# Optimization experiments

Measured on AMD Instinct MI355X. Metric: run time of the kernel, lower is better.

The kernel has to match this reference:

```python
import jax, jax.numpy as jnp
import numpy as np

B, S, H = 2, 2048, 1024
NH, HD = 16, 64  # num_heads, head_size


def setup_inputs() -> dict:
    key = jax.random.key(0)
    ks = jax.random.split(key, 8)
    return {
        "x": jax.random.normal(ks[0], (B, S, H), dtype=jnp.float32),
        "attn_mask": jax.random.randint(ks[1], (B, S, S), 0, 2, dtype=jnp.int32),
        "Wq": jax.random.normal(ks[2], (H, H), dtype=jnp.float32) * 0.02,
        "bq": jax.random.normal(ks[3], (H,), dtype=jnp.float32) * 0.02,
        "Wk": jax.random.normal(ks[4], (H, H), dtype=jnp.float32) * 0.02,
        "bk": jax.random.normal(ks[5], (H,), dtype=jnp.float32) * 0.02,
        "Wv": jax.random.normal(ks[6], (H, H), dtype=jnp.float32) * 0.02,
        "bv": jax.random.normal(ks[7], (H,), dtype=jnp.float32) * 0.02,
    }


def reference(x, attn_mask, Wq, bq, Wk, bk, Wv, bv):
    b, s, h = x.shape
    # QKV projections (self-attention: kv = attention_input)
    q = (jnp.einsum('bih,hx->bix', x, Wq) + bq).reshape(b, s, NH, HD)
    k = (jnp.einsum('bih,hx->bix', x, Wk) + bk).reshape(b, s, NH, HD)
    v = (jnp.einsum('bih,hx->bix', x, Wv) + bv).reshape(b, s, NH, HD)
    scale = 1.0 / (HD ** 0.5)
    # [B, NH, Sq, Skv] score matrix, additive mask, softmax
    attn_score = jnp.einsum('bind,bjnd->bnij', q, k) * scale
    adder = attn_mask.astype(jnp.float32)[:, None, :, :] * -10000.0
    attn_prob = jax.nn.softmax(attn_score + adder, axis=-1)
    # dropout is identity (training=False)
    attn_vec = jnp.einsum('bnij,bjnd->bind', attn_prob, v)
    return attn_vec.reshape(b, s, NH * HD)
```

## Files before the change

### kernel.cpp

```cpp
#include <hip/hip_runtime.h>
#include <hip/hip_bf16.h>
#include <math.h>


#define DI __device__ __forceinline__

typedef unsigned short u16;
typedef unsigned int u32;
typedef unsigned long long u64;
typedef __attribute__((ext_vector_type(8))) short bf16x8;
typedef __attribute__((ext_vector_type(4))) float f32x4;

constexpr int BB = 2, SS = 2048, HH = 1024, NHEAD = 16, HDIM = 64;

DI u16 f2bf(float f) {
  __hip_bfloat16 h = __float2bfloat16(f);
  union { __hip_bfloat16 h; u16 u; } c; c.h = h; return c.u;
}

DI void gload_lds16(const void* g, const void* l) {
  __builtin_amdgcn_global_load_lds(
      (const __attribute__((address_space(1))) u32*)(u64)g,
      (__attribute__((address_space(3))) u32*)(u32)(u64)l,
      16, 0, 0);
}

__global__ void xcast(const float* __restrict__ x, u16* __restrict__ xb) {
  const size_t i = ((size_t)blockIdx.x * 256 + threadIdx.x) * 8;
  float4 f0 = *(const float4*)(x + i);
  float4 f1 = *(const float4*)(x + i + 4);
  bf16x8 v;
  v[0] = (short)f2bf(f0.x); v[1] = (short)f2bf(f0.y);
  v[2] = (short)f2bf(f0.z); v[3] = (short)f2bf(f0.w);
  v[4] = (short)f2bf(f1.x); v[5] = (short)f2bf(f1.y);
  v[6] = (short)f2bf(f1.z); v[7] = (short)f2bf(f1.w);
  *(bf16x8*)(xb + i) = v;
}

__global__ void wtrans(const float* __restrict__ Wq, const float* __restrict__ Wk,
                       const float* __restrict__ Wv, u16* __restrict__ WT) {
  __shared__ u16 tile[64][65];
  const float* W = (blockIdx.z == 0) ? Wq : (blockIdx.z == 1) ? Wk : Wv;
  u16* Wt = WT + (size_t)blockIdx.z * HH * HH;
  const int n0 = blockIdx.x * 64, k0 = blockIdx.y * 64;
  for (int i = threadIdx.x; i < 64 * 64; i += 256) {
    int r = i >> 6, c = i & 63;
    tile[r][c] = f2bf(W[(size_t)(k0 + r) * HH + n0 + c]);
  }
  __syncthreads();
  for (int i = threadIdx.x; i < 64 * 64; i += 256) {
    int r = i >> 6, c = i & 63;
    Wt[(size_t)(n0 + r) * HH + k0 + c] = tile[c][r];
  }
}

__global__ void maskpack(const int* __restrict__ mask, u64* __restrict__ mb) {
  const size_t idx = (size_t)blockIdx.x * 256 + threadIdx.x;
  const int v = mask[idx];
  const u64 bal = __ballot(v != 0);
  if ((threadIdx.x & 63) == 0) mb[idx >> 6] = bal;
}

__global__ __launch_bounds__(256) void qkv_gemm(
    const u16* __restrict__ X, const u16* __restrict__ WTall,
    const float* __restrict__ bq, const float* __restrict__ bk,
    const float* __restrict__ bv,
    u16* __restrict__ Qo, u16* __restrict__ Ko, u16* __restrict__ Vo) {
  __shared__ alignas(128) u16 As[128 * 64];
  __shared__ alignas(128) u16 Bs[128 * 64];

  const int z = blockIdx.z;
  const u16* Wt = WTall + (size_t)z * HH * HH;
  const float* bias = (z == 0) ? bq : (z == 1) ? bk : bv;
  u16* Out = (z == 0) ? Qo : (z == 1) ? Ko : Vo;
  const float oscale = (z == 0) ? 0.18033688011112042f : 1.0f;

  const int tid = threadIdx.x;
  const int lane = tid & 63;
  const int w = tid >> 6;
  const int wm = (w >> 1) * 64, wn = (w & 1) * 64;
  const int lr = lane & 15, lkg = lane >> 4;
  const int m0 = blockIdx.y * 128, n0 = blockIdx.x * 128;

  u32 srow[4], scol[4];
#pragma unroll
  for (int i = 0; i < 4; ++i) {
    u32 f = i * 4096 + w * 1024 + lane * 16;
    u32 g = f ^ (((f >> 7) & 7) << 4);
    srow[i] = g >> 7;
    scol[i] = (g & 127) >> 1;
  }

  u32 aoff[4][2], boff[4][2];
#pragma unroll
  for (int mf = 0; mf < 4; ++mf)
#pragma unroll
    for (int ks = 0; ks < 2; ++ks) {
      int row = wm + mf * 16 + lr;
      aoff[mf][ks] = (u32)((row * 128 + ks * 64 + lkg * 16) ^ ((row & 7) << 4));
      row = wn + mf * 16 + lr;
      boff[mf][ks] = (u32)((row * 128 + ks * 64 + lkg * 16) ^ ((row & 7) << 4));
    }

  f32x4 acc[4][4];
#pragma unroll
  for (int i = 0; i < 4; ++i)
#pragma unroll
    for (int j = 0; j < 4; ++j) acc[i][j] = {0.f, 0.f, 0.f, 0.f};

  const u16* Xb = X + (size_t)m0 * HH;
  const u16* Wb = Wt + (size_t)n0 * HH;

  auto stage = [&](int kt) {
    const int k0 = kt * 64;
#pragma unroll
    for (int i = 0; i < 4; ++i) {
      gload_lds16(Xb + (size_t)srow[i] * HH + k0 + scol[i],
                  (const char*)As + i * 4096 + w * 1024);
      gload_lds16(Wb + (size_t)srow[i] * HH + k0 + scol[i],
                  (const char*)Bs + i * 4096 + w * 1024);
    }
  };

  stage(0);
  const int NT = HH / 64;
  for (int kt = 0; kt < NT; ++kt) {
    __syncthreads();
    bf16x8 a[2][4], bfr[2][4];
#pragma unroll
    for (int ks = 0; ks < 2; ++ks)
#pragma unroll
      for (int i = 0; i < 4; ++i) {
        a[ks][i] = *(const bf16x8*)((const char*)As + aoff[i][ks]);
        bfr[ks][i] = *(const bf16x8*)((const char*)Bs + boff[i][ks]);
      }
    __syncthreads();
    if (kt + 1 < NT) stage(kt + 1);
    __builtin_amdgcn_s_setprio(1);
#pragma unroll
    for (int ks = 0; ks < 2; ++ks)
#pragma unroll
      for (int mf = 0; mf < 4; ++mf)
#pragma unroll
        for (int nf = 0; nf < 4; ++nf)
          acc[mf][nf] = __builtin_amdgcn_mfma_f32_16x16x32_bf16(
              a[ks][mf], bfr[ks][nf], acc[mf][nf], 0, 0, 0);
    __builtin_amdgcn_s_setprio(0);
  }

#pragma unroll
  for (int mf = 0; mf < 4; ++mf)
#pragma unroll
    for (int nf = 0; nf < 4; ++nf) {
      const int gn = n0 + wn + nf * 16 + lr;
      const float bvv = bias[gn];
      const int nh = gn >> 6, hd = gn & 63;
#pragma unroll
      for (int r = 0; r < 4; ++r) {
        const int gm = m0 + wm + mf * 16 + lkg * 4 + r;
        const int bb = gm >> 11, ss = gm & 2047;
        const float v = (acc[mf][nf][r] + bvv) * oscale;
        if (z < 2)
          Out[(((size_t)bb * NHEAD + nh) * SS + ss) * HDIM + hd] = f2bf(v);
        else
          Out[(((size_t)bb * NHEAD + nh) * HDIM + hd) * SS + ss] = f2bf(v);
      }
    }
}

__global__ __launch_bounds__(256) void attn(
    const u16* __restrict__ Q, const u16* __restrict__ K,
    const u16* __restrict__ Vt, const u64* __restrict__ mb,
    float* __restrict__ out) {
  __shared__ alignas(128) u16 Ks[64 * 64];
  __shared__ alignas(128) u16 Vs[64 * 64];
  __shared__ alignas(128) u16 Ps[4][16][72];

  const int nh = blockIdx.x, qt = blockIdx.y, b = blockIdx.z;
  const int bnh = b * NHEAD + nh;
  const u16* Qh = Q + (size_t)bnh * SS * HDIM;
  const u16* Kh = K + (size_t)bnh * SS * HDIM;
  const u16* Vh = Vt + (size_t)bnh * HDIM * SS;
  const int q0 = qt * 64;

  const int tid = threadIdx.x, lane = tid & 63, w = tid >> 6;
  const int lr = lane & 15, lkg = lane >> 4;
  const int qrow_lane = q0 + w * 16 + lr;

  bf16x8 qf[2];
#pragma unroll
  for (int h = 0; h < 2; ++h)
    qf[h] = *(const bf16x8*)(Qh + (size_t)qrow_lane * HDIM + h * 32 + lkg * 8);

  u32 srow[2], scol[2];
#pragma unroll
  for (int i = 0; i < 2; ++i) {
    u32 f = i * 4096 + w * 1024 + lane * 16;
    u32 g = f ^ (((f >> 7) & 7) << 4);
    srow[i] = g >> 7;
    scol[i] = (g & 127) >> 1;
  }

  auto stage = [&](int t) {
    const int kv0 = t * 64;
#pragma unroll
    for (int i = 0; i < 2; ++i) {
      gload_lds16(Kh + (size_t)(kv0 + srow[i]) * HDIM + scol[i],
                  (const char*)Ks + i * 4096 + w * 1024);
      gload_lds16(Vh + (size_t)srow[i] * SS + kv0 + scol[i],
                  (const char*)Vs + i * 4096 + w * 1024);
    }
  };

  u32 koff[4][2];
#pragma unroll
  for (int i = 0; i < 4; ++i)
#pragma unroll
    for (int h = 0; h < 2; ++h) {
      int row = i * 16 + lr;
      koff[i][h] = (u32)((row * 128 + h * 64 + lkg * 16) ^ ((row & 7) << 4));
    }

  bf16x8 ones;
#pragma unroll
  for (int j = 0; j < 8; ++j) ones[j] = (short)0x3F80;

  f32x4 oacc[4];
  f32x4 lacc = {0.f, 0.f, 0.f, 0.f};
#pragma unroll
  for (int n = 0; n < 4; ++n) oacc[n] = {0.f, 0.f, 0.f, 0.f};

  stage(0);
  const int NT = SS / 64;
  for (int t = 0; t < NT; ++t) {
    __syncthreads();

    const u64 sh =
        mb[((size_t)b * SS + qrow_lane) * (SS / 64) + t] >> (lkg * 4);
    const u32 w01 = (u32)sh, w23 = (u32)(sh >> 32);

    f32x4 sacc[4];
#pragma unroll
    for (int kvb = 0; kvb < 4; ++kvb) sacc[kvb] = {0.f, 0.f, 0.f, 0.f};
    __builtin_amdgcn_s_setprio(1);
#pragma unroll
    for (int kvb = 0; kvb < 4; ++kvb)
#pragma unroll
      for (int h = 0; h < 2; ++h) {
        const bf16x8 kf = *(const bf16x8*)((const char*)Ks + koff[kvb][h]);
        sacc[kvb] = __builtin_amdgcn_mfma_f32_16x16x32_bf16(
            kf, qf[h], sacc[kvb], 0, 0, 0);
      }
    __builtin_amdgcn_s_setprio(0);

#pragma unroll
    for (int kvb = 0; kvb < 4; ++kvb) {
      const u32 word = (kvb < 2) ? w01 : w23;
      const int sb = (kvb & 1) * 16;
      union { u16 h[4]; u64 d; } pk;
#pragma unroll
      for (int r = 0; r < 4; ++r) {
        float s = sacc[kvb][r];
        s = ((word >> (sb + r)) & 1u) ? -14000.0f : s;
        pk.h[r] = f2bf(__builtin_amdgcn_exp2f(s));
      }
      *(u64*)&Ps[w][lr][kvb * 16 + lkg * 4] = pk.d;
    }

    __builtin_amdgcn_s_setprio(1);
#pragma unroll
    for (int ks = 0; ks < 2; ++ks) {
      const bf16x8 pf = *(const bf16x8*)&Ps[w][lr][ks * 32 + lkg * 8];
#pragma unroll
      for (int n = 0; n < 4; ++n) {
        const bf16x8 vf = *(const bf16x8*)((const char*)Vs + koff[n][ks]);
        oacc[n] = __builtin_amdgcn_mfma_f32_16x16x32_bf16(
            pf, vf, oacc[n], 0, 0, 0);
      }
      lacc = __builtin_amdgcn_mfma_f32_16x16x32_bf16(pf, ones, lacc, 0, 0, 0);
    }
    __builtin_amdgcn_s_setprio(0);

    __syncthreads();
    if (t + 1 < NT) stage(t + 1);
  }

#pragma unroll
  for (int r = 0; r < 4; ++r) {
    const float rcp = 1.0f / lacc[r];
    const int qrow = q0 + w * 16 + lkg * 4 + r;
#pragma unroll
    for (int n = 0; n < 4; ++n)
      out[((size_t)b * SS + qrow) * HH + nh * HDIM + n * 16 + lr] =
          oacc[n][r] * rcp;
  }
}

extern "C" void kernel_launch(void* const* d_in, const int* in_sizes, int n_in,
                              void* d_out, int out_size, void* d_ws,
                              size_t ws_size, hipStream_t stream) {
  const float* x = (const float*)d_in[0];
  const int* mask = (const int*)d_in[1];
  const float* Wq = (const float*)d_in[2];
  const float* bq = (const float*)d_in[3];
  const float* Wk = (const float*)d_in[4];
  const float* bk = (const float*)d_in[5];
  const float* Wv = (const float*)d_in[6];
  const float* bv = (const float*)d_in[7];
  float* out = (float*)d_out;

  char* ws = (char*)d_ws;
  const size_t MB = 1024 * 1024;
  u16* Qw = (u16*)(ws + 0 * MB);
  u16* Kw = (u16*)(ws + 8 * MB);
  u16* Vtw = (u16*)(ws + 16 * MB);
  u64* mbp = (u64*)(ws + 24 * MB);
  u16* Xb = (u16*)d_out;
  u16* WT = (u16*)((char*)d_out + 8 * MB);

  xcast<<<dim3((BB * SS * HH) / (256 * 8)), 256, 0, stream>>>(x, Xb);
  wtrans<<<dim3(16, 16, 3), 256, 0, stream>>>(Wq, Wk, Wv, WT);
  maskpack<<<dim3((BB * SS * SS) / 256), 256, 0, stream>>>(mask, mbp);
  qkv_gemm<<<dim3(8, 32, 3), 256, 0, stream>>>(Xb, WT, bq, bk, bv, Qw, Kw, Vtw);
  attn<<<dim3(NHEAD, SS / 64, BB), 256, 0, stream>>>(Qw, Kw, Vtw, mbp, out);
}
```

Measured before the change: 133.8 us.

## Load K/V fragments directly from global into registers, dropping LDS staging

The attention kernel no longer stages K and V tiles into shared memory with async global-to-LDS loads and block barriers. Each wave now loads its own MFMA K and V fragments straight from global memory into registers, prefetching K one tile ahead, and both __syncthreads calls are gone. Launch bounds now request 4 blocks per CU to raise occupancy. The trade-off is that every wave re-reads the same K/V data, so global/L1 traffic is about four times higher. V is loaded in the same iteration it is used, leaving little latency hiding, and the final K prefetch reads past the end of the tile range.

Result: slower. 314.2 us (+134.8%).

```diff
diff --git a/kernel.cpp b/kernel.cpp
--- a/kernel.cpp
+++ b/kernel.cpp
@@ -168,13 +168,13 @@
     }
 }
 
-__global__ __launch_bounds__(256) void attn(
+__global__ __launch_bounds__(256, 4) void attn(
     const u16* __restrict__ Q, const u16* __restrict__ K,
     const u16* __restrict__ Vt, const u64* __restrict__ mb,
     float* __restrict__ out) {
-  __shared__ alignas(128) u16 Ks[64 * 64];
-  __shared__ alignas(128) u16 Vs[64 * 64];
-  __shared__ alignas(128) u16 Ps[4][16][72];
+  __shared__ alignas(16) u16 Ps[4][16][72];
+
+  const int tid = threadIdx.x, lane = tid & 63, w = tid >> 6;
 
   const int nh = blockIdx.x, qt = blockIdx.y, b = blockIdx.z;
   const int bnh = b * NHEAD + nh;
@@ -183,7 +183,6 @@
   const u16* Vh = Vt + (size_t)bnh * HDIM * SS;
   const int q0 = qt * 64;
 
-  const int tid = threadIdx.x, lane = tid & 63, w = tid >> 6;
   const int lr = lane & 15, lkg = lane >> 4;
   const int qrow_lane = q0 + w * 16 + lr;
 
@@ -192,35 +191,6 @@
   for (int h = 0; h < 2; ++h)
     qf[h] = *(const bf16x8*)(Qh + (size_t)qrow_lane * HDIM + h * 32 + lkg * 8);
 
-  u32 srow[2], scol[2];
-#pragma unroll
-  for (int i = 0; i < 2; ++i) {
-    u32 f = i * 4096 + w * 1024 + lane * 16;
-    u32 g = f ^ (((f >> 7) & 7) << 4);
-    srow[i] = g >> 7;
-    scol[i] = (g & 127) >> 1;
-  }
-
-  auto stage = [&](int t) {
-    const int kv0 = t * 64;
-#pragma unroll
-    for (int i = 0; i < 2; ++i) {
-      gload_lds16(Kh + (size_t)(kv0 + srow[i]) * HDIM + scol[i],
-                  (const char*)Ks + i * 4096 + w * 1024);
-      gload_lds16(Vh + (size_t)srow[i] * SS + kv0 + scol[i],
-                  (const char*)Vs + i * 4096 + w * 1024);
-    }
-  };
-
-  u32 koff[4][2];
-#pragma unroll
-  for (int i = 0; i < 4; ++i)
-#pragma unroll
-    for (int h = 0; h < 2; ++h) {
-      int row = i * 16 + lr;
-      koff[i][h] = (u32)((row * 128 + h * 64 + lkg * 16) ^ ((row & 7) << 4));
-    }
-
   bf16x8 ones;
 #pragma unroll
   for (int j = 0; j < 8; ++j) ones[j] = (short)0x3F80;
@@ -230,13 +200,34 @@
 #pragma unroll
   for (int n = 0; n < 4; ++n) oacc[n] = {0.f, 0.f, 0.f, 0.f};
 
-  stage(0);
+  bf16x8 kf[4][2], vf[4][2];
+  const u16* Kfl = Kh + (size_t)lr * HDIM + lkg * 8;
+  const u16* Vfl = Vh + (size_t)lr * SS + lkg * 8;
+
+  auto loadK = [&](int t) {
+    const u16* base = Kfl + (size_t)t * 64 * HDIM;
+#pragma unroll
+    for (int i = 0; i < 4; ++i)
+#pragma unroll
+      for (int h = 0; h < 2; ++h)
+        kf[i][h] = *(const bf16x8*)(base + (size_t)i * 16 * HDIM + h * 32);
+  };
+  auto loadV = [&](int t) {
+    const u16* base = Vfl + t * 64;
+#pragma unroll
+    for (int n = 0; n < 4; ++n)
+#pragma unroll
+      for (int h = 0; h < 2; ++h)
+        vf[n][h] = *(const bf16x8*)(base + (size_t)n * 16 * SS + h * 32);
+  };
+
+  const u64* mrow = mb + ((size_t)b * SS + qrow_lane) * (SS / 64);
+
+  loadK(0);
   const int NT = SS / 64;
   for (int t = 0; t < NT; ++t) {
-    __syncthreads();
-
-    const u64 sh =
-        mb[((size_t)b * SS + qrow_lane) * (SS / 64) + t] >> (lkg * 4);
+    loadV(t);
+    const u64 sh = mrow[t] >> (lkg * 4);
     const u32 w01 = (u32)sh, w23 = (u32)(sh >> 32);
 
     f32x4 sacc[4];
@@ -246,12 +237,12 @@
 #pragma unroll
     for (int kvb = 0; kvb < 4; ++kvb)
 #pragma unroll
-      for (int h = 0; h < 2; ++h) {
-        const bf16x8 kf = *(const bf16x8*)((const char*)Ks + koff[kvb][h]);
+      for (int h = 0; h < 2; ++h)
         sacc[kvb] = __builtin_amdgcn_mfma_f32_16x16x32_bf16(
-            kf, qf[h], sacc[kvb], 0, 0, 0);
-      }
+            kf[kvb][h], qf[h], sacc[kvb], 0, 0, 0);
     __builtin_amdgcn_s_setprio(0);
+
+    loadK(t + 1);
 
 #pragma unroll
     for (int kvb = 0; kvb < 4; ++kvb) {
@@ -272,17 +263,12 @@
     for (int ks = 0; ks < 2; ++ks) {
       const bf16x8 pf = *(const bf16x8*)&Ps[w][lr][ks * 32 + lkg * 8];
 #pragma unroll
-      for (int n = 0; n < 4; ++n) {
-        const bf16x8 vf = *(const bf16x8*)((const char*)Vs + koff[n][ks]);
+      for (int n = 0; n < 4; ++n)
         oacc[n] = __builtin_amdgcn_mfma_f32_16x16x32_bf16(
-            pf, vf, oacc[n], 0, 0, 0);
-      }
+            pf, vf[n][ks], oacc[n], 0, 0, 0);
       lacc = __builtin_amdgcn_mfma_f32_16x16x32_bf16(pf, ones, lacc, 0, 0, 0);
     }
     __builtin_amdgcn_s_setprio(0);
-
-    __syncthreads();
-    if (t + 1 < NT) stage(t + 1);
   }
 
 #pragma unroll
```

## Split attention KV range across two wave groups and combine partials in LDS

Applied to the files above, without the earlier changes.

The attention block grows from 256 to 512 threads. Each half of the waves processes half of the KV sequence for the same 64 query rows, each with its own K/V LDS tiles. At the end the second group writes its unnormalized output and row-sum partials to shared memory, and the first group adds them and normalizes. This is split-K within a block, meant to double the parallelism per query tile and halve the serial loop length. The cost is more LDS per block, which may lower occupancy, plus an extra combine step. The combine is valid without max rescaling because the kernel uses no running max.

After: 132.0 us. About the same (-1.3%).

```diff
diff --git a/kernel.cpp b/kernel.cpp
--- a/kernel.cpp
+++ b/kernel.cpp
@@ -168,13 +168,16 @@
     }
 }
 
-__global__ __launch_bounds__(256) void attn(
+__global__ __launch_bounds__(512) void attn(
     const u16* __restrict__ Q, const u16* __restrict__ K,
     const u16* __restrict__ Vt, const u64* __restrict__ mb,
     float* __restrict__ out) {
-  __shared__ alignas(128) u16 Ks[64 * 64];
-  __shared__ alignas(128) u16 Vs[64 * 64];
-  __shared__ alignas(128) u16 Ps[4][16][72];
+  __shared__ alignas(128) char smem[16384 + 16384 + 8 * 16 * 72 * 2];
+  u16* Ks = (u16*)smem;
+  u16* Vs = (u16*)(smem + 16384);
+  typedef u16 PsRow[16][72];
+  PsRow* Ps = (PsRow*)(smem + 32768);
+  float* cmb = (float*)smem;
 
   const int nh = blockIdx.x, qt = blockIdx.y, b = blockIdx.z;
   const int bnh = b * NHEAD + nh;
@@ -184,8 +187,10 @@
   const int q0 = qt * 64;
 
   const int tid = threadIdx.x, lane = tid & 63, w = tid >> 6;
+  const int g = w >> 2, wg = w & 3;
   const int lr = lane & 15, lkg = lane >> 4;
-  const int qrow_lane = q0 + w * 16 + lr;
+  const int qrow_lane = q0 + wg * 16 + lr;
+  const int kvbase = g * (SS / 2);
 
   bf16x8 qf[2];
 #pragma unroll
@@ -195,20 +200,20 @@
   u32 srow[2], scol[2];
 #pragma unroll
   for (int i = 0; i < 2; ++i) {
-    u32 f = i * 4096 + w * 1024 + lane * 16;
-    u32 g = f ^ (((f >> 7) & 7) << 4);
-    srow[i] = g >> 7;
-    scol[i] = (g & 127) >> 1;
+    u32 f = i * 4096 + wg * 1024 + lane * 16;
+    u32 gg = f ^ (((f >> 7) & 7) << 4);
+    srow[i] = gg >> 7;
+    scol[i] = (gg & 127) >> 1;
   }
 
   auto stage = [&](int t) {
-    const int kv0 = t * 64;
+    const int kv0 = kvbase + t * 64;
 #pragma unroll
     for (int i = 0; i < 2; ++i) {
       gload_lds16(Kh + (size_t)(kv0 + srow[i]) * HDIM + scol[i],
-                  (const char*)Ks + i * 4096 + w * 1024);
+                  (const char*)(Ks + g * 4096) + i * 4096 + wg * 1024);
       gload_lds16(Vh + (size_t)srow[i] * SS + kv0 + scol[i],
-                  (const char*)Vs + i * 4096 + w * 1024);
+                  (const char*)(Vs + g * 4096) + i * 4096 + wg * 1024);
     }
   };
 
@@ -231,12 +236,14 @@
   for (int n = 0; n < 4; ++n) oacc[n] = {0.f, 0.f, 0.f, 0.f};
 
   stage(0);
-  const int NT = SS / 64;
+  const int NT = SS / 128;
+  const char* Kbase = (const char*)(Ks + g * 4096);
+  const char* Vbase = (const char*)(Vs + g * 4096);
   for (int t = 0; t < NT; ++t) {
     __syncthreads();
 
     const u64 sh =
-        mb[((size_t)b * SS + qrow_lane) * (SS / 64) + t] >> (lkg * 4);
+        mb[((size_t)b * SS + qrow_lane) * (SS / 64) + g * NT + t] >> (lkg * 4);
     const u32 w01 = (u32)sh, w23 = (u32)(sh >> 32);
 
     f32x4 sacc[4];
@@ -247,7 +254,7 @@
     for (int kvb = 0; kvb < 4; ++kvb)
 #pragma unroll
       for (int h = 0; h < 2; ++h) {
-        const bf16x8 kf = *(const bf16x8*)((const char*)Ks + koff[kvb][h]);
+        const bf16x8 kf = *(const bf16x8*)(Kbase + koff[kvb][h]);
         sacc[kvb] = __builtin_amdgcn_mfma_f32_16x16x32_bf16(
             kf, qf[h], sacc[kvb], 0, 0, 0);
       }
@@ -273,7 +280,7 @@
       const bf16x8 pf = *(const bf16x8*)&Ps[w][lr][ks * 32 + lkg * 8];
 #pragma unroll
       for (int n = 0; n < 4; ++n) {
-        const bf16x8 vf = *(const bf16x8*)((const char*)Vs + koff[n][ks]);
+        const bf16x8 vf = *(const bf16x8*)(Vbase + koff[n][ks]);
         oacc[n] = __builtin_amdgcn_mfma_f32_16x16x32_bf16(
             pf, vf, oacc[n], 0, 0, 0);
       }
@@ -285,14 +292,28 @@
     if (t + 1 < NT) stage(t + 1);
   }
 
-#pragma unroll
-  for (int r = 0; r < 4; ++r) {
-    const float rcp = 1.0f / lacc[r];
-    const int qrow = q0 + w * 16 + lkg * 4 + r;
+  const int lid = wg * 64 + lane;
+  if (g == 1) {
 #pragma unroll
     for (int n = 0; n < 4; ++n)
-      out[((size_t)b * SS + qrow) * HH + nh * HDIM + n * 16 + lr] =
-          oacc[n][r] * rcp;
+#pragma unroll
+      for (int r = 0; r < 4; ++r) cmb[(n * 4 + r) * 256 + lid] = oacc[n][r];
+#pragma unroll
+    for (int r = 0; r < 4; ++r) cmb[(16 + r) * 256 + lid] = lacc[r];
+  }
+  __syncthreads();
+  if (g == 0) {
+#pragma unroll
+    for (int r = 0; r < 4; ++r) {
+      const float l = lacc[r] + cmb[(16 + r) * 256 + lid];
+      const float rcp = 1.0f / l;
+      const int qrow = q0 + wg * 16 + lkg * 4 + r;
+#pragma unroll
+      for (int n = 0; n < 4; ++n) {
+        const float o = oacc[n][r] + cmb[(n * 4 + r) * 256 + lid];
+        out[((size_t)b * SS + qrow) * HH + nh * HDIM + n * 16 + lr] = o * rcp;
+      }
+    }
   }
 }
 
@@ -322,5 +343,5 @@
   wtrans<<<dim3(16, 16, 3), 256, 0, stream>>>(Wq, Wk, Wv, WT);
   maskpack<<<dim3((BB * SS * SS) / 256), 256, 0, stream>>>(mask, mbp);
   qkv_gemm<<<dim3(8, 32, 3), 256, 0, stream>>>(Xb, WT, bq, bk, bv, Qw, Kw, Vtw);
-  attn<<<dim3(NHEAD, SS / 64, BB), 256, 0, stream>>>(Qw, Kw, Vtw, mbp, out);
-}
+  attn<<<dim3(NHEAD, SS / 64, BB), 512, 0, stream>>>(Qw, Kw, Vtw, mbp, out);
+}
```
